# Kernel tuning notes

Hardware: AMD Instinct MI355X
Metric: run time of the kernel (lower is better)

Reference implementation:

```python
import jax, jax.numpy as jnp
import numpy as np

B = 2048      # env batch (graphs)
A = 8         # agents per graph (fully connected)
N = B * A     # total nodes
DIN = 192     # raw obs dim
HD = 256      # h_dim (base MLP)
MD = 256      # mem_dim (GRU)
GD = 128      # gnn_dim (per-head GATv2 out, concat=False -> head mean)
H = 4         # GAT heads
NA = 20       # n_actions
ED = 3        # edge_dim


def setup_inputs() -> dict:
    key = jax.random.key(0)
    ks = jax.random.split(key, 16)
    # fully-connected directed graph per group of A agents, no self loops
    s, d = np.meshgrid(np.arange(A), np.arange(A), indexing='ij')
    mask = s != d
    s = s[mask]; d = d[mask]                     # [A*(A-1)]
    off = (np.arange(B) * A)[:, None]
    src = (off + s[None, :]).reshape(-1)
    dst = (off + d[None, :]).reshape(-1)
    edge_index = jnp.asarray(np.stack([src, dst]), dtype=jnp.int32)  # [2, E]
    E = src.shape[0]
    p = lambda k, sh: jax.random.normal(ks[k], sh, jnp.float32) * 0.02
    return {
        'inputs': jax.random.normal(ks[0], (N, DIN), jnp.float32),
        'hidden_states': jax.random.normal(ks[1], (N, MD), jnp.float32) * 0.1,
        'edge_index': edge_index,
        'edge_attr': jax.random.uniform(ks[2], (E, ED), jnp.float32),
        # base MLP (2 layers: Linear+ReLU+LayerNorm)
        'W1': p(3, (DIN, HD)), 'b1': jnp.zeros(HD), 'g1': jnp.ones(HD), 'be1': jnp.zeros(HD),
        'W2': p(4, (HD, HD)),  'b2': jnp.zeros(HD), 'g2': jnp.ones(HD), 'be2': jnp.zeros(HD),
        # GRUCell
        'Wih': p(5, (3 * MD, HD)), 'Whh': p(6, (3 * MD, MD)),
        'bih': jnp.zeros(3 * MD), 'bhh': jnp.zeros(3 * MD),
        # GATv2Conv (edge_dim=3, heads=4, concat=False, residual)
        'Wl': p(7, (MD, H * GD)), 'bl': jnp.zeros(H * GD),
        'Wr': p(8, (MD, H * GD)), 'br': jnp.zeros(H * GD),
        'att': p(9, (H, GD)),
        'We': p(10, (ED, H * GD)),
        'Wres': p(11, (MD, GD)),
        'bg': jnp.zeros(GD),
        # head: LayerNorm + Linear
        'lng': jnp.ones(GD), 'lnb': jnp.zeros(GD),
        'Wout': p(12, (GD, NA)), 'bout': jnp.zeros(NA),
    }


def _ln(x, g, b):
    mu = jnp.mean(x, -1, keepdims=True)
    xc = x - mu
    v = jnp.mean(xc * xc, -1, keepdims=True)
    return xc * jax.lax.rsqrt(v + 1e-5) * g + b


def _fwd(inputs, hidden_states, edge_attr, edge_index,
         W1, b1, g1, be1, W2, b2, g2, be2,
         Wih, Whh, bih, bhh,
         Wl, bl, Wr, br, att, We, Wres, bg,
         lng, lnb, Wout, bout):
    src, dst = edge_index[0], edge_index[1]
    # ---- base MLP encode ----
    x = _ln(jax.nn.relu(inputs @ W1 + b1), g1, be1)
    x = _ln(jax.nn.relu(x @ W2 + b2), g2, be2)          # [N, HD]
    # ---- SimpleConv(aggr='mean', combine_root='self_loop') ----
    s = jax.ops.segment_sum(x[src], dst, num_segments=N) + x
    deg = jax.ops.segment_sum(jnp.ones(src.shape[0], x.dtype), dst, num_segments=N) + 1.0
    x = s / deg[:, None]                                 # [N, HD]
    # ---- GRUCell ----
    gi = x @ Wih.T + bih
    gh = hidden_states @ Whh.T + bhh
    ir, iz, inn = jnp.split(gi, 3, -1)
    hr, hz, hn = jnp.split(gh, 3, -1)
    r = jax.nn.sigmoid(ir + hr)
    z = jax.nn.sigmoid(iz + hz)
    n = jnp.tanh(inn + r * hn)
    h = (1.0 - z) * n + z * hidden_states                # [N, MD]
    # ---- GATv2Conv (add self loops, edge_attr fill='mean') ----
    loop = jnp.arange(N, dtype=src.dtype)
    sf = jnp.concatenate([src, loop])
    df = jnp.concatenate([dst, loop])
    ea = jnp.concatenate([edge_attr, jnp.broadcast_to(edge_attr.mean(0), (N, ED))], 0)
    xl = (h @ Wl + bl).reshape(N, H, GD)
    xr = (h @ Wr + br).reshape(N, H, GD)
    m = xl[sf] + xr[df] + (ea @ We).reshape(-1, H, GD)   # [Ef, H, GD]
    m = jnp.where(m > 0, m, 0.2 * m)                     # leaky_relu(0.2)
    logits = jnp.einsum('ehc,hc->eh', m, att)            # [Ef, H]
    mx = jax.ops.segment_max(logits, df, num_segments=N)
    ex = jnp.exp(logits - mx[df])
    den = jax.ops.segment_sum(ex, df, num_segments=N)
    alpha = ex / (den[df] + 1e-16)                       # segment softmax
    out = jax.ops.segment_sum(xl[sf] * alpha[..., None], df, num_segments=N)
    out = out.mean(1) + h @ Wres + bg                    # head mean + residual + bias
    zg = jax.nn.relu(out)                                # [N, GD]
    # ---- action head ----
    q = _ln(zg, lng, lnb) @ Wout + bout                  # [N, NA]
    return q, h


def reference(inputs, hidden_states, edge_index, edge_attr,
              W1, b1, g1, be1, W2, b2, g2, be2,
              Wih, Whh, bih, bhh,
              Wl, bl, Wr, br, att, We, Wres, bg,
              lng, lnb, Wout, bout):
    return _fwd(inputs, hidden_states, edge_attr, edge_index,
                W1, b1, g1, be1, W2, b2, g2, be2,
                Wih, Whh, bih, bhh,
                Wl, bl, Wr, br, att, We, Wres, bg,
                lng, lnb, Wout, bout)
```

## Files before the change

### kernel.cpp

```cpp
#include <hip/hip_runtime.h>
#include <hip/hip_bf16.h>

constexpr int NB  = 2048;
constexpr int AG  = 8;
constexpr int NN  = NB * AG;
constexpr int DIN = 192;
constexpr int HD  = 256;
constexpr int MD  = 256;
constexpr int GD  = 128;
constexpr int NA  = 20;
constexpr int NE  = NB * AG * (AG - 1);

typedef __attribute__((ext_vector_type(8))) short bfrag8;
typedef __attribute__((ext_vector_type(4))) short sfrag4;
typedef __attribute__((ext_vector_type(4))) float f32x4;

#define MFMA16(a, b, c) __builtin_amdgcn_mfma_f32_16x16x32_bf16((a), (b), (c), 0, 0, 0)

#define GLOAD_LDS16(g, l) __builtin_amdgcn_global_load_lds(                  \
    (const __attribute__((address_space(1))) void*)(g),                      \
    (__attribute__((address_space(3))) void*)(l), 16, 0, 0)

__device__ __forceinline__ float bf2f(__hip_bfloat16 x) { return __bfloat162float(x); }
__device__ __forceinline__ __hip_bfloat16 f2bf(float x) { return __float2bfloat16(x); }
__device__ __forceinline__ short f2bs(float x) {
    __hip_bfloat16 b = __float2bfloat16(x);
    return *reinterpret_cast<short*>(&b);
}
__device__ __forceinline__ bfrag8 ldf(const __hip_bfloat16* p) { return *(const bfrag8*)p; }
__device__ __forceinline__ bfrag8 ldf32(const float* p) {
    const f32x4 a = *(const f32x4*)p;
    const f32x4 b = *(const f32x4*)(p + 4);
    bfrag8 r;
    r[0] = f2bs(a[0]); r[1] = f2bs(a[1]); r[2] = f2bs(a[2]); r[3] = f2bs(a[3]);
    r[4] = f2bs(b[0]); r[5] = f2bs(b[1]); r[6] = f2bs(b[2]); r[7] = f2bs(b[3]);
    return r;
}
__device__ __forceinline__ float sigmf(float x) { return 1.f / (1.f + __expf(-x)); }
__device__ __forceinline__ float blo(unsigned u) { return __uint_as_float(u << 16); }
__device__ __forceinline__ float bhi(unsigned u) { return __uint_as_float(u & 0xffff0000u); }

__global__ __launch_bounds__(256) void k_prep(
    const float* __restrict__ W1, const float* __restrict__ W2,
    const float* __restrict__ Wih, const float* __restrict__ Whh,
    const float* __restrict__ Wl, const float* __restrict__ bl,
    const float* __restrict__ Wr, const float* __restrict__ br,
    const float* __restrict__ Wres, const float* __restrict__ Wout,
    const float* __restrict__ ea,
    __hip_bfloat16* __restrict__ W1T, __hip_bfloat16* __restrict__ W2T,
    __hip_bfloat16* __restrict__ WihB, __hip_bfloat16* __restrict__ WhhB,
    __hip_bfloat16* __restrict__ WcatT, float* __restrict__ WoutTf,
    float* __restrict__ bcat, float* __restrict__ ea_partials)
{
    __shared__ float sw[4][3];
    const int tid = threadIdx.x;
    if (blockIdx.x >= 3151) {
        const int b = blockIdx.x - 3151;
        float a0 = 0.f, a1 = 0.f, a2 = 0.f;
#pragma unroll
        for (int k = 0; k < 7; k++) {
            int e = b * 1792 + k * 256 + tid;
            a0 += ea[e * 3 + 0];
            a1 += ea[e * 3 + 1];
            a2 += ea[e * 3 + 2];
        }
#pragma unroll
        for (int off = 1; off < 64; off <<= 1) {
            a0 += __shfl_xor(a0, off); a1 += __shfl_xor(a1, off); a2 += __shfl_xor(a2, off);
        }
        if ((tid & 63) == 0) { sw[tid >> 6][0] = a0; sw[tid >> 6][1] = a1; sw[tid >> 6][2] = a2; }
        __syncthreads();
        if (tid == 0) {
            ea_partials[b * 3 + 0] = sw[0][0] + sw[1][0] + sw[2][0] + sw[3][0];
            ea_partials[b * 3 + 1] = sw[0][1] + sw[1][1] + sw[2][1] + sw[3][1];
            ea_partials[b * 3 + 2] = sw[0][2] + sw[1][2] + sw[2][2] + sw[3][2];
        }
        return;
    }
    int i = blockIdx.x * 256 + tid;
    if (i < 49152) { int o = i / 192, c = i % 192; W1T[i] = f2bf(W1[c * 256 + o]); return; }
    i -= 49152;
    if (i < 65536) { int o = i >> 8, c = i & 255; W2T[i] = f2bf(W2[c * 256 + o]); return; }
    i -= 65536;
    if (i < 196608) { WihB[i] = f2bf(Wih[i]); return; }
    i -= 196608;
    if (i < 196608) { WhhB[i] = f2bf(Whh[i]); return; }
    i -= 196608;
    if (i < 294912) {
        int o = i >> 8, c = i & 255;
        float v;
        if (o < 512)       v = Wl[c * 512 + o];
        else if (o < 1024) v = Wr[c * 512 + (o - 512)];
        else               v = Wres[c * 128 + (o - 1024)];
        WcatT[i] = f2bf(v); return;
    }
    i -= 294912;
    if (i < 2560) { int o = i >> 7, c = i & 127; WoutTf[i] = Wout[c * 20 + o]; return; }
    i -= 2560;
    if (i < 1152) {
        float v = 0.f;
        if (i < 512) v = bl[i]; else if (i < 1024) v = br[i - 512];
        bcat[i] = v;
    }
}

__global__ __launch_bounds__(256) void k_encode(
    const float* __restrict__ in,
    const __hip_bfloat16* __restrict__ W1T,
    const float* __restrict__ b1, const float* __restrict__ g1, const float* __restrict__ be1,
    const __hip_bfloat16* __restrict__ W2T,
    const float* __restrict__ b2, const float* __restrict__ g2, const float* __restrict__ be2,
    __hip_bfloat16* __restrict__ xm)
{
    __shared__ float sf[16][257];
    __shared__ alignas(16) __hip_bfloat16 sb[16][264];
    const int tid = threadIdx.x;
    const int lane = tid & 63, w = tid >> 6;
    const int r = lane & 15, q = lane >> 4;
    const int m0 = blockIdx.x * 16;

    {
        bfrag8 af[6];
        const float* ap = in + (size_t)(m0 + r) * DIN + q * 8;
#pragma unroll
        for (int kb = 0; kb < 6; kb++) af[kb] = ldf32(ap + kb * 32);
#pragma unroll
        for (int i = 0; i < 4; i++) {
            int t = w * 4 + i;
            const __hip_bfloat16* wp = W1T + (size_t)(t * 16 + r) * DIN + q * 8;
            bfrag8 bf[6];
#pragma unroll
            for (int kb = 0; kb < 6; kb++) bf[kb] = ldf(wp + kb * 32);
            f32x4 acc = (f32x4){0.f, 0.f, 0.f, 0.f};
#pragma unroll
            for (int kb = 0; kb < 6; kb++) acc = MFMA16(af[kb], bf[kb], acc);
            int col = t * 16 + r;
            float bias = b1[col];
#pragma unroll
            for (int reg = 0; reg < 4; reg++)
                sf[q * 4 + reg][col] = fmaxf(acc[reg] + bias, 0.f);
        }
    }
    __syncthreads();
    {
        int rowi = tid >> 4, c16 = tid & 15;
        float vals[16]; float s = 0.f, s2 = 0.f;
#pragma unroll
        for (int j = 0; j < 16; j++) { float v = sf[rowi][c16 + 16 * j]; vals[j] = v; s += v; s2 += v * v; }
#pragma unroll
        for (int off = 1; off < 16; off <<= 1) { s += __shfl_xor(s, off); s2 += __shfl_xor(s2, off); }
        float mean = s * (1.f / HD);
        float var = fmaxf(s2 * (1.f / HD) - mean * mean, 0.f);
        float rs = rsqrtf(var + 1e-5f);
#pragma unroll
        for (int j = 0; j < 16; j++) {
            int col = c16 + 16 * j;
            sb[rowi][col] = f2bf((vals[j] - mean) * rs * g1[col] + be1[col]);
        }
    }
    __syncthreads();

    {
        bfrag8 af[8];
        const __hip_bfloat16* ap = &sb[r][0];
#pragma unroll
        for (int kb = 0; kb < 8; kb++) af[kb] = ldf(ap + kb * 32 + q * 8);
        float outv[4][4];
#pragma unroll
        for (int i = 0; i < 4; i++) {
            int t = w * 4 + i;
            const __hip_bfloat16* wp = W2T + (size_t)(t * 16 + r) * HD + q * 8;
            bfrag8 bf[8];
#pragma unroll
            for (int kb = 0; kb < 8; kb++) bf[kb] = ldf(wp + kb * 32);
            f32x4 acc = (f32x4){0.f, 0.f, 0.f, 0.f};
#pragma unroll
            for (int kb = 0; kb < 8; kb++) acc = MFMA16(af[kb], bf[kb], acc);
#pragma unroll
            for (int reg = 0; reg < 4; reg++) outv[i][reg] = acc[reg];
        }
        __syncthreads();
#pragma unroll
        for (int i = 0; i < 4; i++) {
            int col = (w * 4 + i) * 16 + r;
            float bias = b2[col];
#pragma unroll
            for (int reg = 0; reg < 4; reg++)
                sf[q * 4 + reg][col] = fmaxf(outv[i][reg] + bias, 0.f);
        }
    }
    __syncthreads();
    {
        int rowi = tid >> 4, c16 = tid & 15;
        float vals[16]; float s = 0.f, s2 = 0.f;
#pragma unroll
        for (int j = 0; j < 16; j++) { float v = sf[rowi][c16 + 16 * j]; vals[j] = v; s += v; s2 += v * v; }
#pragma unroll
        for (int off = 1; off < 16; off <<= 1) { s += __shfl_xor(s, off); s2 += __shfl_xor(s2, off); }
        float mean = s * (1.f / HD);
        float var = fmaxf(s2 * (1.f / HD) - mean * mean, 0.f);
        float rs = rsqrtf(var + 1e-5f);
#pragma unroll
        for (int j = 0; j < 16; j++) {
            int col = c16 + 16 * j;
            sb[rowi][col] = f2bf((vals[j] - mean) * rs * g2[col] + be2[col]);
        }
    }
    __syncthreads();
    {
        int col = tid;
        float a0 = 0.f, a1 = 0.f;
#pragma unroll
        for (int i = 0; i < 8; i++) { a0 += bf2f(sb[i][col]); a1 += bf2f(sb[8 + i][col]); }
        xm[(size_t)(2 * blockIdx.x) * HD + col] = f2bf(a0 * 0.125f);
        xm[(size_t)(2 * blockIdx.x + 1) * HD + col] = f2bf(a1 * 0.125f);
    }
}

__global__ __launch_bounds__(256) void k_gi(
    const __hip_bfloat16* __restrict__ xm,
    const __hip_bfloat16* __restrict__ WihB,
    const float* __restrict__ bih,
    float* __restrict__ gi)
{
    const int tid = threadIdx.x;
    const int lane = tid & 63, w = tid >> 6;
    const int r = lane & 15, q = lane >> 4;
    const int m0 = (blockIdx.x >> 1) * 16;
    const int t0 = (blockIdx.x & 1) * 24;

    bfrag8 af[8];
    const __hip_bfloat16* ap = xm + (size_t)(m0 + r) * MD + q * 8;
#pragma unroll
    for (int kb = 0; kb < 8; kb++) af[kb] = ldf(ap + kb * 32);
#pragma unroll
    for (int i = 0; i < 6; i++) {
        int t = t0 + w * 6 + i;
        const __hip_bfloat16* wp = WihB + (size_t)(t * 16 + r) * MD + q * 8;
        bfrag8 bf[8];
#pragma unroll
        for (int kb = 0; kb < 8; kb++) bf[kb] = ldf(wp + kb * 32);
        f32x4 acc = (f32x4){0.f, 0.f, 0.f, 0.f};
#pragma unroll
        for (int kb = 0; kb < 8; kb++) acc = MFMA16(af[kb], bf[kb], acc);
        int col = t * 16 + r;
        float bias = bih[col];
#pragma unroll
        for (int reg = 0; reg < 4; reg++) {
            int R = m0 + q * 4 + reg;
            gi[(size_t)R * 768 + col] = acc[reg] + bias;
        }
    }
}

__global__ __launch_bounds__(256, 2) void k_gruG(
    const float* __restrict__ hprev,
    const __hip_bfloat16* __restrict__ WhhB,
    const float* __restrict__ bhh,
    const float* __restrict__ gi,
    float* __restrict__ hout)
{
    const int tid = threadIdx.x;
    const int lane = tid & 63, w = tid >> 6;
    const int r = lane & 15, q = lane >> 4;
    const int bswz = (blockIdx.x & 7) * 64 + (blockIdx.x >> 3);
    const int m0 = (bswz >> 2) * 128;
    const int cg = (bswz & 3) * 64;

    bfrag8 afr[2][8];
#pragma unroll
    for (int t = 0; t < 2; t++) {
        const float* ap = hprev + (size_t)(m0 + (w * 2 + t) * 16 + r) * MD + q * 8;
#pragma unroll
        for (int kb = 0; kb < 8; kb++) afr[t][kb] = ldf32(ap + kb * 32);
    }
    f32x4 acc[2][12];
#pragma unroll
    for (int t = 0; t < 2; t++)
#pragma unroll
        for (int n = 0; n < 12; n++) acc[t][n] = (f32x4){0.f, 0.f, 0.f, 0.f};

#pragma unroll
    for (int kb = 0; kb < 8; kb++) {
        bfrag8 bfB[12];
#pragma unroll
        for (int g = 0; g < 3; g++)
#pragma unroll
            for (int nj = 0; nj < 4; nj++)
                bfB[g * 4 + nj] = ldf(WhhB + (size_t)(g * 256 + cg + nj * 16 + r) * MD
                                      + kb * 32 + q * 8);
#pragma unroll
        for (int t = 0; t < 2; t++)
#pragma unroll
            for (int n = 0; n < 12; n++)
                acc[t][n] = MFMA16(bfB[n], afr[t][kb], acc[t][n]);
    }

#pragma unroll
    for (int t = 0; t < 2; t++) {
        int node = m0 + (w * 2 + t) * 16 + r;
        const float* gir = gi + (size_t)(node >> 3) * 768;
#pragma unroll
        for (int nj = 0; nj < 4; nj++) {
            int c = cg + nj * 16 + q * 4;
            f32x4 gR = *(const f32x4*)&gir[c];
            f32x4 gZ = *(const f32x4*)&gir[256 + c];
            f32x4 gN = *(const f32x4*)&gir[512 + c];
            f32x4 bR = *(const f32x4*)&bhh[c];
            f32x4 bZ = *(const f32x4*)&bhh[256 + c];
            f32x4 bN = *(const f32x4*)&bhh[512 + c];
            f32x4 hp = *(const f32x4*)&hprev[(size_t)node * MD + c];
            f32x4 hv;
#pragma unroll
            for (int reg = 0; reg < 4; reg++) {
                float rr = sigmf(gR[reg] + acc[t][0 + nj][reg] + bR[reg]);
                float zz = sigmf(gZ[reg] + acc[t][4 + nj][reg] + bZ[reg]);
                float nn = tanhf(gN[reg] + rr * (acc[t][8 + nj][reg] + bN[reg]));
                hv[reg] = (1.f - zz) * nn + zz * hp[reg];
            }
            *(f32x4*)&hout[(size_t)node * MD + c] = hv;
        }
    }
}

__global__ __launch_bounds__(256, 2) void k_xlr(
    const float* __restrict__ h,
    const __hip_bfloat16* __restrict__ WcatT,
    const float* __restrict__ bcat,
    __hip_bfloat16* __restrict__ xlr)
{
    __shared__ alignas(16) __hip_bfloat16 sB[128 * 64];
    const int tid = threadIdx.x;
    const int lane = tid & 63, w = tid >> 6;
    const int r = lane & 15, q = lane >> 4;
    const int wm = w >> 1, wn = w & 1;

    const int lin = (blockIdx.x & 7) * 144 + (blockIdx.x >> 3);
    const int m0 = (lin / 9) * 128;
    const int nb = (lin % 9) * 128;

    const int srow = tid >> 3;
    const int sch  = (tid & 7) ^ (srow & 7);

    f32x4 acc[4][4];
#pragma unroll
    for (int am = 0; am < 4; am++)
#pragma unroll
        for (int bn = 0; bn < 4; bn++) acc[am][bn] = (f32x4){0.f, 0.f, 0.f, 0.f};

    for (int kt = 0; kt < 4; ++kt) {
        if (kt) __syncthreads();
#pragma unroll
        for (int i = 0; i < 4; ++i) {
            const __hip_bfloat16* gp = WcatT + (size_t)(nb + i * 32 + srow) * 256
                                       + kt * 64 + sch * 8;
            GLOAD_LDS16(gp, &sB[i * 2048 + tid * 8]);
        }
        __syncthreads();

#pragma unroll
        for (int kk = 0; kk < 2; ++kk) {
            bfrag8 af[4], bf[4];
#pragma unroll
            for (int am = 0; am < 4; ++am)
                af[am] = ldf32(h + (size_t)(m0 + wm * 64 + am * 16 + r) * MD
                               + kt * 64 + kk * 32 + q * 8);
#pragma unroll
            for (int bn = 0; bn < 4; ++bn) {
                const int R = wn * 64 + bn * 16 + r;
                const int c = (kk * 4 + q) ^ (R & 7);
                bf[bn] = *(const bfrag8*)&sB[R * 64 + c * 8];
            }
#pragma unroll
            for (int am = 0; am < 4; ++am)
#pragma unroll
                for (int bn = 0; bn < 4; ++bn)
                    acc[am][bn] = MFMA16(bf[bn], af[am], acc[am][bn]);
        }
    }

#pragma unroll
    for (int bn = 0; bn < 4; ++bn) {
        const int fb = nb + wn * 64 + bn * 16 + q * 4;
        const f32x4 bv = *(const f32x4*)&bcat[fb];
#pragma unroll
        for (int am = 0; am < 4; ++am) {
            const int node = m0 + wm * 64 + am * 16 + r;
            sfrag4 pk;
#pragma unroll
            for (int reg = 0; reg < 4; reg++) pk[reg] = f2bs(acc[am][bn][reg] + bv[reg]);
            *(sfrag4*)&xlr[(size_t)node * 1152 + fb] = pk;
        }
    }
}

__global__ __launch_bounds__(256) void k_gat(
    const __hip_bfloat16* __restrict__ xlr,
    const float* __restrict__ ea,
    const float* __restrict__ ea_partials,
    const float* __restrict__ att,
    const float* __restrict__ We,
    const float* __restrict__ bg,
    const float* __restrict__ lng, const float* __restrict__ lnb,
    const float* __restrict__ WoutTf,
    const float* __restrict__ bout,
    float* __restrict__ qout)
{
    __shared__ alignas(16) __hip_bfloat16 sx[16][1160];
    __shared__ alignas(16) float szg[16][136];
    __shared__ float slog[2][4][8][8];
    __shared__ float smean[4];
    const int tid = threadIdx.x;
    const int lane = tid & 63, w = tid >> 6;
    const int r = lane & 15, q = lane >> 4;
    const int m0 = blockIdx.x * 16;

    if (tid < 3) {
        float s = 0.f;
        for (int i = 0; i < 64; i++) s += ea_partials[i * 3 + tid];
        smean[tid] = s * (1.f / NE);
    }
    for (int idx = tid; idx < 2304; idx += 256) {
        int row = idx / 144, off = (idx % 144) * 8;
        *(uint4*)&sx[row][off] = *(const uint4*)&xlr[(size_t)(m0 + row) * 1152 + off];
    }

    float vea[2][3];
    {
        int l = (lane < 56) ? lane : 0;
#pragma unroll
        for (int g = 0; g < 2; g++) {
            const float* ep = ea + (size_t)((blockIdx.x * 2 + g) * 56 + l) * 3;
            vea[g][0] = ep[0]; vea[g][1] = ep[1]; vea[g][2] = ep[2];
        }
    }
    __syncthreads();
    const float em0 = smean[0], em1 = smean[1], em2 = smean[2];

    {
        const int li = lane & 31, half = lane >> 5;
#pragma unroll
        for (int t = 0; t < 2; t++) {
            const int combo = w * 2 + t;
            const int gg = combo >> 2, hh = combo & 3;
            const f32x4 va  = *(const f32x4*)&att[hh * 128 + li * 4];
            const f32x4 vw0 = *(const f32x4*)&We[0 * 512 + hh * 128 + li * 4];
            const f32x4 vw1 = *(const f32x4*)&We[1 * 512 + hh * 128 + li * 4];
            const f32x4 vw2 = *(const f32x4*)&We[2 * 512 + hh * 128 + li * 4];
            float at0 = va[0],  at1 = va[1],  at2 = va[2],  at3 = va[3];
            float w00 = vw0[0], w01 = vw0[1], w02 = vw0[2], w03 = vw0[3];
            float w10 = vw1[0], w11 = vw1[1], w12 = vw1[2], w13 = vw1[3];
            float w20 = vw2[0], w21 = vw2[1], w22 = vw2[2], w23 = vw2[3];
            float ve0 = vea[gg][0], ve1 = vea[gg][1], ve2 = vea[gg][2];
            float xv[4][4];
#pragma unroll
            for (int sh2 = 0; sh2 < 4; sh2++) {
                int sL = sh2 * 2 + half;
                uint2 uxl = *(const uint2*)&sx[gg * 8 + sL][hh * 128 + li * 4];
                xv[sh2][0] = blo(uxl.x); xv[sh2][1] = bhi(uxl.x);
                xv[sh2][2] = blo(uxl.y); xv[sh2][3] = bhi(uxl.y);
            }
            float mylog = 0.f;
#pragma unroll
            for (int d = 0; d < 8; d++) {
                uint2 uxr = *(const uint2*)&sx[gg * 8 + d][512 + hh * 128 + li * 4];
                float xr0 = blo(uxr.x), xr1 = bhi(uxr.x), xr2 = blo(uxr.y), xr3 = bhi(uxr.y);
#pragma unroll
                for (int sh2 = 0; sh2 < 4; sh2++) {
                    int sL = sh2 * 2 + half;
                    int el = sL * 7 + d - (d > sL ? 1 : 0);
                    float e0 = __shfl(ve0, el), e1 = __shfl(ve1, el), e2 = __shfl(ve2, el);
                    bool slf = (sL == d);
                    e0 = slf ? em0 : e0; e1 = slf ? em1 : e1; e2 = slf ? em2 : e2;
                    float p, m;
                    m = fmaf(e2, w20, fmaf(e1, w10, fmaf(e0, w00, xv[sh2][0]))) + xr0;
                    m = fmaxf(m, 0.2f * m); p = m * at0;
                    m = fmaf(e2, w21, fmaf(e1, w11, fmaf(e0, w01, xv[sh2][1]))) + xr1;
                    m = fmaxf(m, 0.2f * m); p = fmaf(m, at1, p);
                    m = fmaf(e2, w22, fmaf(e1, w12, fmaf(e0, w02, xv[sh2][2]))) + xr2;
                    m = fmaxf(m, 0.2f * m); p = fmaf(m, at2, p);
                    m = fmaf(e2, w23, fmaf(e1, w13, fmaf(e0, w03, xv[sh2][3]))) + xr3;
                    m = fmaxf(m, 0.2f * m); p = fmaf(m, at3, p);
                    p += __shfl_xor(p, 1);  p += __shfl_xor(p, 2);  p += __shfl_xor(p, 4);
                    p += __shfl_xor(p, 8);  p += __shfl_xor(p, 16);
                    float got = __shfl(p, ((lane & 1) << 5) | li);
                    bool want = ((lane >> 3) == d) && (((lane & 7) >> 1) == sh2);
                    mylog = want ? got : mylog;
                }
            }
            ((float*)&slog[gg][hh][0][0])[lane] = mylog;
        }
    }
    __syncthreads();

    if (tid < 64) {
        int sg = tid >> 5, sh2 = (tid >> 3) & 3, d = tid & 7;
        float* L = &slog[sg][sh2][d][0];
        float mx = L[0];
#pragma unroll
        for (int s = 1; s < 8; s++) mx = fmaxf(mx, L[s]);
        float ex[8]; float den = 0.f;
#pragma unroll
        for (int s = 0; s < 8; s++) { ex[s] = __expf(L[s] - mx); den += ex[s]; }
        float inv = 1.f / (den + 1e-16f);
#pragma unroll
        for (int s = 0; s < 8; s++) L[s] = ex[s] * inv;
    }
    __syncthreads();

    {
        f32x4 acc0 = (f32x4){0.f, 0.f, 0.f, 0.f};
        f32x4 acc1 = (f32x4){0.f, 0.f, 0.f, 0.f};
        const int ggr = r >> 3, dr = r & 7;
#pragma unroll
        for (int ah = 0; ah < 4; ah++) {
            bfrag8 afA;
#pragma unroll
            for (int j = 0; j < 8; j++) {
                int k = q * 8 + j;
                float v = 0.f;
                if (k < 16) {
                    int ggk = k >> 3, s = k & 7;
                    if (ggk == ggr) v = slog[ggk][ah][dr][s];
                }
                afA[j] = f2bs(v);
            }
#pragma unroll
            for (int j2 = 0; j2 < 2; j2++) {
                int chunk = w * 2 + j2;
                bfrag8 bfB;
#pragma unroll
                for (int j = 0; j < 8; j++) {
                    int k = (q * 8 + j) & 15;
                    bfB[j] = *(const short*)&sx[k][ah * 128 + chunk * 16 + r];
                }
                if (j2 == 0) acc0 = MFMA16(afA, bfB, acc0);
                else         acc1 = MFMA16(afA, bfB, acc1);
            }
        }
#pragma unroll
        for (int j2 = 0; j2 < 2; j2++) {
            f32x4 a = j2 ? acc1 : acc0;
            int c = (w * 2 + j2) * 16 + r;
            float bgc = bg[c];
#pragma unroll
            for (int reg = 0; reg < 4; reg++) {
                int row = q * 4 + reg;
                float o = a[reg] * 0.25f + bf2f(sx[row][1024 + c]) + bgc;
                szg[row][c] = fmaxf(o, 0.f);
            }
        }
    }
    __syncthreads();

    {
        int row = tid >> 4, j = tid & 15;
        float v[8]; float s = 0.f, s2 = 0.f;
#pragma unroll
        for (int cj = 0; cj < 8; cj++) { v[cj] = szg[row][j + 16 * cj]; s += v[cj]; s2 += v[cj] * v[cj]; }
#pragma unroll
        for (int off = 1; off < 16; off <<= 1) { s += __shfl_xor(s, off); s2 += __shfl_xor(s2, off); }
        float mean = s * (1.f / GD);
        float var = fmaxf(s2 * (1.f / GD) - mean * mean, 0.f);
        float rs = rsqrtf(var + 1e-5f);
#pragma unroll
        for (int cj = 0; cj < 8; cj++) {
            int c = j + 16 * cj;
            szg[row][c] = (v[cj] - mean) * rs * lng[c] + lnb[c];
        }
    }
    __syncthreads();

    {
        int row = tid >> 4, j = tid & 15;
        for (int jj = j; jj < NA; jj += 16) {
            float a = bout[jj];
            const float* wo = WoutTf + jj * 128;
#pragma unroll
            for (int c4 = 0; c4 < 32; c4++) {
                f32x4 z = *(const f32x4*)&szg[row][c4 * 4];
                const f32x4 wv = *(const f32x4*)&wo[c4 * 4];
                a = fmaf(z[0], wv[0], a); a = fmaf(z[1], wv[1], a);
                a = fmaf(z[2], wv[2], a); a = fmaf(z[3], wv[3], a);
            }
            qout[(size_t)(m0 + row) * NA + jj] = a;
        }
    }
}

extern "C" void kernel_launch(void* const* d_in, const int* in_sizes, int n_in,
                              void* d_out, int out_size, void* d_ws, size_t ws_size,
                              hipStream_t stream) {
    const float* inp   = (const float*)d_in[0];
    const float* hid   = (const float*)d_in[1];
    const float* eatt  = (const float*)d_in[3];
    const float* W1    = (const float*)d_in[4];
    const float* b1    = (const float*)d_in[5];
    const float* g1    = (const float*)d_in[6];
    const float* be1   = (const float*)d_in[7];
    const float* W2    = (const float*)d_in[8];
    const float* b2    = (const float*)d_in[9];
    const float* g2    = (const float*)d_in[10];
    const float* be2   = (const float*)d_in[11];
    const float* Wih   = (const float*)d_in[12];
    const float* Whh   = (const float*)d_in[13];
    const float* bih   = (const float*)d_in[14];
    const float* bhh   = (const float*)d_in[15];
    const float* Wl    = (const float*)d_in[16];
    const float* bl    = (const float*)d_in[17];
    const float* Wr    = (const float*)d_in[18];
    const float* br    = (const float*)d_in[19];
    const float* att   = (const float*)d_in[20];
    const float* We    = (const float*)d_in[21];
    const float* Wres  = (const float*)d_in[22];
    const float* bg    = (const float*)d_in[23];
    const float* lng   = (const float*)d_in[24];
    const float* lnb   = (const float*)d_in[25];
    const float* Wout  = (const float*)d_in[26];
    const float* bout  = (const float*)d_in[27];

    float* qout = (float*)d_out;
    float* hout = (float*)d_out + (size_t)NN * NA;

    char* ws = (char*)d_ws;
    float*           ea_partials = (float*)ws;
    __hip_bfloat16*  xm    = (__hip_bfloat16*)(ws + 2048);
    float*           gi    = (float*)(ws + 1050624);
    __hip_bfloat16*  W1T   = (__hip_bfloat16*)(ws + 7342080);
    __hip_bfloat16*  W2T   = (__hip_bfloat16*)(ws + 7440384);
    __hip_bfloat16*  WihB  = (__hip_bfloat16*)(ws + 7571456);
    __hip_bfloat16*  WhhB  = (__hip_bfloat16*)(ws + 7964672);
    __hip_bfloat16*  WcatT = (__hip_bfloat16*)(ws + 8357888);
    float*           bcat  = (float*)(ws + 8947712);
    float*           WoutTf= (float*)(ws + 8952320);
    __hip_bfloat16*  xlr   = (__hip_bfloat16*)(ws + 8962560);

    k_prep<<<3215, 256, 0, stream>>>(W1, W2, Wih, Whh, Wl, bl, Wr, br, Wres, Wout, eatt,
                                     W1T, W2T, WihB, WhhB, WcatT, WoutTf, bcat, ea_partials);
    k_encode<<<NN / 16, 256, 0, stream>>>(inp, W1T, b1, g1, be1, W2T, b2, g2, be2, xm);
    k_gi<<<256, 256, 0, stream>>>(xm, WihB, bih, gi);
    k_gruG<<<512, 256, 0, stream>>>(hid, WhhB, bhh, gi, hout);
    k_xlr<<<1152, 256, 0, stream>>>(hout, WcatT, bcat, xlr);
    k_gat<<<NN / 16, 256, 0, stream>>>(xlr, eatt, ea_partials, att, We, bg,
                                       lng, lnb, WoutTf, bout, qout);
}
```

Baseline: 316.9 us.

## Remap GAT attention logits to one edge per lane and alias shared buffers

Reassigns the attention-logit computation so each lane owns one (src,dst) edge pair and loops over the 128 channels of its head, instead of each lane owning 4 channels with a 5-step shuffle reduction per edge. The segment softmax is folded into the same warp via xor-shuffles across the 8 source lanes, which removes a separate single-wave softmax phase and one barrier. The sx and szg shared buffers are aliased to cut LDS footprint, which requires an extra barrier before writing szg. The new per-lane loop reads att/We vectors through the cache and issues wide LDS reads that may bank-conflict.

```diff
diff --git a/kernel.cpp b/kernel.cpp
--- a/kernel.cpp
+++ b/kernel.cpp
@@ -406,10 +406,11 @@
     const float* __restrict__ bout,
     float* __restrict__ qout)
 {
-    __shared__ alignas(16) __hip_bfloat16 sx[16][1160];
-    __shared__ alignas(16) float szg[16][136];
+    __shared__ alignas(16) char smem_raw[16 * 1160 * 2];
     __shared__ float slog[2][4][8][8];
     __shared__ float smean[4];
+    __hip_bfloat16 (*sx)[1160] = (__hip_bfloat16 (*)[1160])smem_raw;
+    float (*szg)[136] = (float (*)[136])smem_raw;
     const int tid = threadIdx.x;
     const int lane = tid & 63, w = tid >> 6;
     const int r = lane & 15, q = lane >> 4;
@@ -425,86 +426,67 @@
         *(uint4*)&sx[row][off] = *(const uint4*)&xlr[(size_t)(m0 + row) * 1152 + off];
     }
 
-    float vea[2][3];
-    {
-        int l = (lane < 56) ? lane : 0;
-#pragma unroll
-        for (int g = 0; g < 2; g++) {
-            const float* ep = ea + (size_t)((blockIdx.x * 2 + g) * 56 + l) * 3;
-            vea[g][0] = ep[0]; vea[g][1] = ep[1]; vea[g][2] = ep[2];
-        }
-    }
-    __syncthreads();
-    const float em0 = smean[0], em1 = smean[1], em2 = smean[2];
-
-    {
-        const int li = lane & 31, half = lane >> 5;
+    const int sL = lane & 7, dL = lane >> 3;
+    const int gg = w >> 1;
+    float e0 = 0.f, e1 = 0.f, e2 = 0.f;
+    if (sL != dL) {
+        int eidx = sL * 7 + dL - (dL > sL ? 1 : 0);
+        const float* ep = ea + (size_t)((blockIdx.x * 2 + gg) * 56 + eidx) * 3;
+        e0 = ep[0]; e1 = ep[1]; e2 = ep[2];
+    }
+    __syncthreads();
+    if (sL == dL) { e0 = smean[0]; e1 = smean[1]; e2 = smean[2]; }
+
+    {
+        const __hip_bfloat16* xlrow = &sx[gg * 8 + sL][0];
+        const __hip_bfloat16* xrrow = &sx[gg * 8 + dL][512];
 #pragma unroll
         for (int t = 0; t < 2; t++) {
-            const int combo = w * 2 + t;
-            const int gg = combo >> 2, hh = combo & 3;
-            const f32x4 va  = *(const f32x4*)&att[hh * 128 + li * 4];
-            const f32x4 vw0 = *(const f32x4*)&We[0 * 512 + hh * 128 + li * 4];
-            const f32x4 vw1 = *(const f32x4*)&We[1 * 512 + hh * 128 + li * 4];
-            const f32x4 vw2 = *(const f32x4*)&We[2 * 512 + hh * 128 + li * 4];
-            float at0 = va[0],  at1 = va[1],  at2 = va[2],  at3 = va[3];
-            float w00 = vw0[0], w01 = vw0[1], w02 = vw0[2], w03 = vw0[3];
-            float w10 = vw1[0], w11 = vw1[1], w12 = vw1[2], w13 = vw1[3];
-            float w20 = vw2[0], w21 = vw2[1], w22 = vw2[2], w23 = vw2[3];
-            float ve0 = vea[gg][0], ve1 = vea[gg][1], ve2 = vea[gg][2];
-            float xv[4][4];
-#pragma unroll
-            for (int sh2 = 0; sh2 < 4; sh2++) {
-                int sL = sh2 * 2 + half;
-                uint2 uxl = *(const uint2*)&sx[gg * 8 + sL][hh * 128 + li * 4];
-                xv[sh2][0] = blo(uxl.x); xv[sh2][1] = bhi(uxl.x);
-                xv[sh2][2] = blo(uxl.y); xv[sh2][3] = bhi(uxl.y);
+            const int hh = (w & 1) * 2 + t;
+            const int woff = __builtin_amdgcn_readfirstlane(hh * 128);
+            const float* attp = att + woff;
+            const float* w0p = We + woff;
+            const float* w1p = We + 512 + woff;
+            const float* w2p = We + 1024 + woff;
+            const __hip_bfloat16* xlp = xlrow + hh * 128;
+            const __hip_bfloat16* xrp = xrrow + hh * 128;
+            float p0 = 0.f, p1 = 0.f;
+#pragma unroll 4
+            for (int cb = 0; cb < 16; cb++) {
+                const uint4 uxl = *(const uint4*)&xlp[cb * 8];
+                const uint4 uxr = *(const uint4*)&xrp[cb * 8];
+                const f32x4 a0  = *(const f32x4*)&attp[cb * 8];
+                const f32x4 a1  = *(const f32x4*)&attp[cb * 8 + 4];
+                const f32x4 w00 = *(const f32x4*)&w0p[cb * 8];
+                const f32x4 w01 = *(const f32x4*)&w0p[cb * 8 + 4];
+                const f32x4 w10 = *(const f32x4*)&w1p[cb * 8];
+                const f32x4 w11 = *(const f32x4*)&w1p[cb * 8 + 4];
+                const f32x4 w20 = *(const f32x4*)&w2p[cb * 8];
+                const f32x4 w21 = *(const f32x4*)&w2p[cb * 8 + 4];
+                float mm;
+#define CH1(XL, XR, WA, WB, WC, AT, ACC)                                          \
+                mm = fmaf(e2, (WC), fmaf(e1, (WB), fmaf(e0, (WA), (XL)))) + (XR); \
+                mm = fmaxf(mm, 0.2f * mm); ACC = fmaf(mm, (AT), ACC);
+                CH1(blo(uxl.x), blo(uxr.x), w00[0], w10[0], w20[0], a0[0], p0)
+                CH1(bhi(uxl.x), bhi(uxr.x), w00[1], w10[1], w20[1], a0[1], p1)
+                CH1(blo(uxl.y), blo(uxr.y), w00[2], w10[2], w20[2], a0[2], p0)
+                CH1(bhi(uxl.y), bhi(uxr.y), w00[3], w10[3], w20[3], a0[3], p1)
+                CH1(blo(uxl.z), blo(uxr.z), w01[0], w11[0], w21[0], a1[0], p0)
+                CH1(bhi(uxl.z), bhi(uxr.z), w01[1], w11[1], w21[1], a1[1], p1)
+                CH1(blo(uxl.w), blo(uxr.w), w01[2], w11[2], w21[2], a1[2], p0)
+                CH1(bhi(uxl.w), bhi(uxr.w), w01[3], w11[3], w21[3], a1[3], p1)
+#undef CH1
             }
-            float mylog = 0.f;
-#pragma unroll
-            for (int d = 0; d < 8; d++) {
-                uint2 uxr = *(const uint2*)&sx[gg * 8 + d][512 + hh * 128 + li * 4];
-                float xr0 = blo(uxr.x), xr1 = bhi(uxr.x), xr2 = blo(uxr.y), xr3 = bhi(uxr.y);
-#pragma unroll
-                for (int sh2 = 0; sh2 < 4; sh2++) {
-                    int sL = sh2 * 2 + half;
-                    int el = sL * 7 + d - (d > sL ? 1 : 0);
-                    float e0 = __shfl(ve0, el), e1 = __shfl(ve1, el), e2 = __shfl(ve2, el);
-                    bool slf = (sL == d);
-                    e0 = slf ? em0 : e0; e1 = slf ? em1 : e1; e2 = slf ? em2 : e2;
-                    float p, m;
-                    m = fmaf(e2, w20, fmaf(e1, w10, fmaf(e0, w00, xv[sh2][0]))) + xr0;
-                    m = fmaxf(m, 0.2f * m); p = m * at0;
-                    m = fmaf(e2, w21, fmaf(e1, w11, fmaf(e0, w01, xv[sh2][1]))) + xr1;
-                    m = fmaxf(m, 0.2f * m); p = fmaf(m, at1, p);
-                    m = fmaf(e2, w22, fmaf(e1, w12, fmaf(e0, w02, xv[sh2][2]))) + xr2;
-                    m = fmaxf(m, 0.2f * m); p = fmaf(m, at2, p);
-                    m = fmaf(e2, w23, fmaf(e1, w13, fmaf(e0, w03, xv[sh2][3]))) + xr3;
-                    m = fmaxf(m, 0.2f * m); p = fmaf(m, at3, p);
-                    p += __shfl_xor(p, 1);  p += __shfl_xor(p, 2);  p += __shfl_xor(p, 4);
-                    p += __shfl_xor(p, 8);  p += __shfl_xor(p, 16);
-                    float got = __shfl(p, ((lane & 1) << 5) | li);
-                    bool want = ((lane >> 3) == d) && (((lane & 7) >> 1) == sh2);
-                    mylog = want ? got : mylog;
-                }
-            }
-            ((float*)&slog[gg][hh][0][0])[lane] = mylog;
-        }
-    }
-    __syncthreads();
-
-    if (tid < 64) {
-        int sg = tid >> 5, sh2 = (tid >> 3) & 3, d = tid & 7;
-        float* L = &slog[sg][sh2][d][0];
-        float mx = L[0];
-#pragma unroll
-        for (int s = 1; s < 8; s++) mx = fmaxf(mx, L[s]);
-        float ex[8]; float den = 0.f;
-#pragma unroll
-        for (int s = 0; s < 8; s++) { ex[s] = __expf(L[s] - mx); den += ex[s]; }
-        float inv = 1.f / (den + 1e-16f);
-#pragma unroll
-        for (int s = 0; s < 8; s++) L[s] = ex[s] * inv;
+            float p = p0 + p1;
+            float mx = fmaxf(p, __shfl_xor(p, 1));
+            mx = fmaxf(mx, __shfl_xor(mx, 2));
+            mx = fmaxf(mx, __shfl_xor(mx, 4));
+            float exv = __expf(p - mx);
+            float den = exv + __shfl_xor(exv, 1);
+            den += __shfl_xor(den, 2);
+            den += __shfl_xor(den, 4);
+            ((float*)&slog[gg][hh][0][0])[lane] = exv / (den + 1e-16f);
+        }
     }
     __syncthreads();
 
@@ -538,6 +520,7 @@
                 else         acc1 = MFMA16(afA, bfB, acc1);
             }
         }
+        float ov[8];
 #pragma unroll
         for (int j2 = 0; j2 < 2; j2++) {
             f32x4 a = j2 ? acc1 : acc0;
@@ -547,8 +530,16 @@
             for (int reg = 0; reg < 4; reg++) {
                 int row = q * 4 + reg;
                 float o = a[reg] * 0.25f + bf2f(sx[row][1024 + c]) + bgc;
-                szg[row][c] = fmaxf(o, 0.f);
+                ov[j2 * 4 + reg] = fmaxf(o, 0.f);
             }
+        }
+        __syncthreads();
+#pragma unroll
+        for (int j2 = 0; j2 < 2; j2++) {
+            int c = (w * 2 + j2) * 16 + r;
+#pragma unroll
+            for (int reg = 0; reg < 4; reg++)
+                szg[q * 4 + reg][c] = ov[j2 * 4 + reg];
         }
     }
     __syncthreads();
```

Result: no change. 314.3 us (-0.8%).
